# Performance work log

Hardware: AMD Instinct MI355X
Metric: run time of the kernel (lower is better)

Reference implementation:

```python
import jax, jax.numpy as jnp
import numpy as np

HIDDEN = 2048
NUM_HEADS = 16
HEAD_DIM = HIDDEN // NUM_HEADS  # 128
ROPE_THETA = 10000.0
T = 4096


def _rope(x, positions):
    # x: [T, H, D]; neox-style rotary (rotate halves), matching vLLM get_rope default
    half = HEAD_DIM // 2
    inv_freq = 1.0 / (ROPE_THETA ** (jnp.arange(0, half, dtype=jnp.float32) / half))
    freqs = positions.astype(jnp.float32)[:, None] * inv_freq[None, :]  # [T, half]
    cos = jnp.cos(freqs)[:, None, :]  # [T, 1, half]
    sin = jnp.sin(freqs)[:, None, :]
    x1, x2 = x[..., :half], x[..., half:]
    return jnp.concatenate([x1 * cos - x2 * sin, x2 * cos + x1 * sin], axis=-1)


def setup_inputs() -> dict:
    key = jax.random.key(0)
    k1, k2, k3 = jax.random.split(key, 3)
    return {
        "hidden_states": jax.random.normal(k1, (T, HIDDEN), dtype=jnp.float32),
        "positions": jnp.arange(T, dtype=jnp.int32),
        "w_qkv": jax.random.normal(k2, (HIDDEN, 3 * HIDDEN), dtype=jnp.float32) * (HIDDEN ** -0.5),
        "w_o": jax.random.normal(k3, (HIDDEN, HIDDEN), dtype=jnp.float32) * (HIDDEN ** -0.5),
    }


def reference(hidden_states, positions, w_qkv, w_o):
    qkv = hidden_states @ w_qkv  # [T, 3H]
    q, k, v = jnp.split(qkv, 3, axis=-1)
    q = q.reshape(T, NUM_HEADS, HEAD_DIM)
    k = k.reshape(T, NUM_HEADS, HEAD_DIM)
    v = v.reshape(T, NUM_HEADS, HEAD_DIM)
    q = _rope(q, positions)
    k = _rope(k, positions)
    scale = HEAD_DIM ** -0.5
    # causal SDPA over flattened single sequence
    scores = jnp.einsum("qhd,khd->hqk", q, k) * scale  # [H, T, T]
    causal = jnp.tril(jnp.ones((T, T), dtype=bool))
    scores = jnp.where(causal[None, :, :], scores, jnp.finfo(scores.dtype).min)
    probs = jax.nn.softmax(scores, axis=-1)
    attn = jnp.einsum("hqk,khd->qhd", probs, v).reshape(T, HIDDEN)
    return attn @ w_o
```

## Files before the change

### kernel.cpp

```cpp
#include <hip/hip_runtime.h>
#include <hip/hip_bf16.h>
#include <cstdint>
#include <cstddef>

#define T_SEQ 4096
#define HID   2048
#define NH    16
#define HD    128
#define QKVN  6144
#define KVB   32
#define CHT   16
#define CPH   144

typedef unsigned short u16;
typedef unsigned int u32;
typedef __bf16 bf16x8 __attribute__((ext_vector_type(8)));
typedef float  f32x4  __attribute__((ext_vector_type(4)));

typedef const __attribute__((address_space(1))) void* gas_ptr;
typedef __attribute__((address_space(3))) void* las_ptr;

__device__ __forceinline__ void async16(const void* g, void* l) {
  __builtin_amdgcn_global_load_lds((gas_ptr)g, (las_ptr)l, 16, 0, 0);
}

__device__ __forceinline__ u16 f2bf(float f) {
  unsigned int u = __float_as_uint(f);
  u += 0x7fffu + ((u >> 16) & 1u);
  return (u16)(u >> 16);
}

__device__ __forceinline__ float bf2f(u16 x) {
  return __uint_as_float((unsigned)x << 16);
}

__global__ void cast_f32_bf16(const float* __restrict__ in, u16* __restrict__ out, int n) {
  int i = (blockIdx.x * blockDim.x + threadIdx.x) * 4;
  if (i >= n) return;
  float4 v = *(const float4*)&in[i];
  uint2 o;
  o.x = (unsigned)f2bf(v.x) | ((unsigned)f2bf(v.y) << 16);
  o.y = (unsigned)f2bf(v.z) | ((unsigned)f2bf(v.w) << 16);
  *(uint2*)&out[i] = o;
}

__global__ void transpose_cast(const float* __restrict__ in, u16* __restrict__ out,
                               int R, int C) {
  __shared__ float tile[64][65];
  int c0 = blockIdx.x * 64, r0 = blockIdx.y * 64;
  int tid = threadIdx.x;
#pragma unroll
  for (int i = 0; i < 16; ++i) {
    int e = i * 256 + tid;
    int rr = e >> 6, cc = e & 63;
    tile[rr][cc] = in[(size_t)(r0 + rr) * C + c0 + cc];
  }
  __syncthreads();
#pragma unroll
  for (int i = 0; i < 16; ++i) {
    int e = i * 256 + tid;
    int oc = e >> 6, orr = e & 63;
    out[(size_t)(c0 + oc) * R + r0 + orr] = f2bf(tile[orr][oc]);
  }
}

template <typename OUT>
__global__ __launch_bounds__(256)
void gemm_bf16_bt(const u16* __restrict__ A, const u16* __restrict__ BT,
                  OUT* __restrict__ C, int M, int N, int K) {
  __shared__ u16 As[2][128 * 32];
  __shared__ u16 Bs[2][128 * 32];
  int tid = threadIdx.x;
  int row0 = blockIdx.y * 128, col0 = blockIdx.x * 128;
  int wv = tid >> 6, lane = tid & 63, lr = lane & 15, lq = lane >> 4;
  int wm = (wv >> 1) * 64, wn = (wv & 1) * 64;
  f32x4 acc[4][4] = {};

  auto stage = [&](int buf, int ks) {
#pragma unroll
    for (int k = 0; k < 2; ++k) {
      int c = k * 256 + tid;
      int row = c >> 2, col = c & 3;
      int key = (row >> 1) & 3;
      async16(&A[(size_t)(row0 + row) * K + ks + (col ^ key) * 8], &As[buf][c * 8]);
      async16(&BT[(size_t)(col0 + row) * K + ks + (col ^ key) * 8], &Bs[buf][c * 8]);
    }
  };

  stage(0, 0);
  __syncthreads();
  int nk = K >> 5;
  for (int t = 0; t < nk; ++t) {
    int cur = t & 1;
    if (t + 1 < nk) stage(cur ^ 1, (t + 1) * 32);

    const char* AsB = (const char*)&As[cur][0];
    const char* BsB = (const char*)&Bs[cur][0];
    bf16x8 a[4], b[4];
#pragma unroll
    for (int mi = 0; mi < 4; ++mi) {
      int row = wm + mi * 16 + lr;
      a[mi] = *(const bf16x8*)(AsB + row * 64 + ((lq ^ ((row >> 1) & 3)) << 4));
    }
#pragma unroll
    for (int ni = 0; ni < 4; ++ni) {
      int row = wn + ni * 16 + lr;
      b[ni] = *(const bf16x8*)(BsB + row * 64 + ((lq ^ ((row >> 1) & 3)) << 4));
    }
#pragma unroll
    for (int mi = 0; mi < 4; ++mi)
#pragma unroll
      for (int ni = 0; ni < 4; ++ni)
        acc[mi][ni] = __builtin_amdgcn_mfma_f32_16x16x32_bf16(a[mi], b[ni], acc[mi][ni], 0, 0, 0);
    __syncthreads();
  }

#pragma unroll
  for (int mi = 0; mi < 4; ++mi)
#pragma unroll
    for (int ni = 0; ni < 4; ++ni)
#pragma unroll
      for (int r = 0; r < 4; ++r) {
        float v = acc[mi][ni][r];
        size_t idx = (size_t)(row0 + wm + mi * 16 + lq * 4 + r) * N + col0 + wn + ni * 16 + lr;
        if constexpr (sizeof(OUT) == 2) C[idx] = (OUT)f2bf(v);
        else                            C[idx] = (OUT)v;
      }
}

#define SCL2 0.12753224f

__global__ void rope_reorg(const u16* __restrict__ qkv, const int* __restrict__ pos,
                           u16* __restrict__ Qh, u16* __restrict__ Kh) {
  int idx = blockIdx.x * 256 + threadIdx.x;
  if (idx >= T_SEQ * NH * 64) return;
  int d = idx & 63;
  int h = (idx >> 6) & (NH - 1);
  int t = idx >> 10;
  float p = (float)pos[t];
  float inv = exp2f((float)d * -0.20762050594046932f);
  float f = p * inv;
  float s, c;
  __sincosf(f, &s, &c);

  size_t ib = (size_t)t * QKVN + h * HD + d;
  float q1 = bf2f(qkv[ib]), q2 = bf2f(qkv[ib + 64]);
  float k1 = bf2f(qkv[ib + HID]), k2 = bf2f(qkv[ib + HID + 64]);
  size_t ob = ((size_t)h * T_SEQ + t) * HD + d;
  Qh[ob]      = f2bf((q1 * c - q2 * s) * SCL2);
  Qh[ob + 64] = f2bf((q2 * c + q1 * s) * SCL2);
  Kh[ob]      = f2bf(k1 * c - k2 * s);
  Kh[ob + 64] = f2bf(k2 * c + k1 * s);
}

__global__ void vtrans(const u16* __restrict__ qkv, u16* __restrict__ Vt) {
  __shared__ u16 tile[64][136];
  int t0 = blockIdx.x * 64;
  int h = blockIdx.y;
  int tid = threadIdx.x;
#pragma unroll
  for (int i = 0; i < 32; ++i) {
    int e = i * 256 + tid;
    int tt = e >> 7, d = e & 127;
    tile[tt][d] = qkv[(size_t)(t0 + tt) * QKVN + 2 * HID + h * HD + d];
  }
  __syncthreads();
#pragma unroll
  for (int i = 0; i < 32; ++i) {
    int e = i * 256 + tid;
    int d = e >> 6, tt = e & 63;
    Vt[((size_t)h * HD + d) * T_SEQ + t0 + tt] = tile[tt][d];
  }
}

__global__ __launch_bounds__(256)
void attn_fwd(const u16* __restrict__ Qh, const u16* __restrict__ Kh,
              const u16* __restrict__ Vt, u16* __restrict__ Opart,
              float2* __restrict__ ml) {
  __shared__ u16 Ks[2][32 * 128];
  __shared__ u16 Vs[2][128 * 32];
  __shared__ u16 Ps[4][32 * 32];

  int tid = threadIdx.x;
  int wv = tid >> 6, lane = tid & 63, lr = lane & 15, lq = lane >> 4;
  char* PsB = (char*)&Ps[wv][0];

  int id = blockIdx.x;
  int h = id / CPH;
  int w = id - h * CPH;
  int bq = 0, acc = 0;
  for (;;) {
    int ch = (bq + 4) >> 2;
    if (w < acc + ch) break;
    acc += ch;
    ++bq;
  }
  int c = w - acc;
  int nt = 4 * bq + 4;
  int j0 = c * CHT, j1 = min(j0 + CHT, nt);
  int q0 = bq * 128, wrow0 = q0 + wv * 32;

  bf16x8 qf[2][4];
#pragma unroll
  for (int qi = 0; qi < 2; ++qi)
#pragma unroll
    for (int kd = 0; kd < 4; ++kd)
      qf[qi][kd] = *(const bf16x8*)
          &Qh[((size_t)h * T_SEQ + wrow0 + qi * 16 + lr) * HD + kd * 32 + lq * 8];

  f32x4 acc_o[2][8] = {};
  float m_run[2] = {-1e30f, -1e30f};
  float l_run[2] = {0.0f, 0.0f};

  auto stage = [&](int buf, int jb) {
#pragma unroll
    for (int k = 0; k < 2; ++k) {
      int cc = k * 256 + tid;
      int row = cc >> 4;
      int sc = (cc ^ (row & 7)) & 15;
      async16(&Kh[((size_t)h * T_SEQ + jb + row) * HD + sc * 8], &Ks[buf][cc * 8]);
    }
#pragma unroll
    for (int k = 0; k < 2; ++k) {
      int cc = k * 256 + tid;
      int row = cc >> 2, col = cc & 3;
      int key = (row >> 1) & 3;
      async16(&Vt[((size_t)h * HD + row) * T_SEQ + jb + (col ^ key) * 8],
              &Vs[buf][cc * 8]);
    }
  };

  stage(0, j0 * KVB);
  __syncthreads();

  for (int j = j0; j < j1; ++j) {
    int cur = (j - j0) & 1;
    int jb = j * KVB;
    if (j + 1 < j1) stage(cur ^ 1, jb + KVB);

    if (jb <= wrow0 + 31) {
      const char* KsB = (const char*)&Ks[cur][0];
      const char* VsB = (const char*)&Vs[cur][0];

      f32x4 st[2][2] = {};
#pragma unroll
      for (int kd = 0; kd < 4; ++kd) {
#pragma unroll
        for (int kj = 0; kj < 2; ++kj) {
          int row = kj * 16 + lr;
          int byt = (row << 8) + kd * 64 + lq * 16;
          bf16x8 kf = *(const bf16x8*)(KsB + (byt ^ ((row & 7) << 4)));
#pragma unroll
          for (int qi = 0; qi < 2; ++qi)
            st[kj][qi] = __builtin_amdgcn_mfma_f32_16x16x32_bf16(
                kf, qf[qi][kd], st[kj][qi], 0, 0, 0);
        }
      }

      if (jb + KVB - 1 > wrow0) {
#pragma unroll
        for (int qi = 0; qi < 2; ++qi) {
          int qg = wrow0 + qi * 16 + lr;
#pragma unroll
          for (int kj = 0; kj < 2; ++kj)
#pragma unroll
            for (int r = 0; r < 4; ++r)
              if (jb + kj * 16 + lq * 4 + r > qg) st[kj][qi][r] = -1e30f;
        }
      }

      float sf[2];
#pragma unroll
      for (int qi = 0; qi < 2; ++qi) {
        float mx = fmaxf(fmaxf(fmaxf(st[0][qi][0], st[0][qi][1]),
                               fmaxf(st[0][qi][2], st[0][qi][3])),
                         fmaxf(fmaxf(st[1][qi][0], st[1][qi][1]),
                               fmaxf(st[1][qi][2], st[1][qi][3])));
        mx = fmaxf(mx, __shfl_xor(mx, 16));
        mx = fmaxf(mx, __shfl_xor(mx, 32));
        float mnew = fmaxf(m_run[qi], mx);
        sf[qi] = exp2f(m_run[qi] - mnew);
        m_run[qi] = mnew;

        int rowb = (qi * 16 + lr) * 64;
        int key = ((lr >> 1) & 3) << 4;
        float rs = 0.0f;
#pragma unroll
        for (int kj = 0; kj < 2; ++kj) {
          float p0 = exp2f(st[kj][qi][0] - mnew);
          float p1 = exp2f(st[kj][qi][1] - mnew);
          float p2 = exp2f(st[kj][qi][2] - mnew);
          float p3 = exp2f(st[kj][qi][3] - mnew);
          rs += (p0 + p1) + (p2 + p3);
          uint2 wq;
          wq.x = (u32)f2bf(p0) | ((u32)f2bf(p1) << 16);
          wq.y = (u32)f2bf(p2) | ((u32)f2bf(p3) << 16);
          *(uint2*)(PsB + rowb + (((kj * 16 + lq * 4) * 2) ^ key)) = wq;
        }
        l_run[qi] = l_run[qi] * sf[qi] + rs;
      }

#pragma unroll
      for (int mi = 0; mi < 2; ++mi) {
        float sfb[4];
#pragma unroll
        for (int r = 0; r < 4; ++r) sfb[r] = __shfl(sf[mi], lq * 4 + r);
#pragma unroll
        for (int nd = 0; nd < 8; ++nd)
#pragma unroll
          for (int r = 0; r < 4; ++r) acc_o[mi][nd][r] *= sfb[r];
      }

#pragma unroll
      for (int mi = 0; mi < 2; ++mi) {
        int prow = mi * 16 + lr;
        bf16x8 pa = *(const bf16x8*)(PsB + prow * 64 + ((lq ^ ((lr >> 1) & 3)) << 4));
#pragma unroll
        for (int nd = 0; nd < 8; ++nd) {
          int vrow = nd * 16 + lr;
          bf16x8 vb = *(const bf16x8*)(VsB + vrow * 64 + ((lq ^ ((vrow >> 1) & 3)) << 4));
          acc_o[mi][nd] = __builtin_amdgcn_mfma_f32_16x16x32_bf16(
              pa, vb, acc_o[mi][nd], 0, 0, 0);
        }
      }
    }
    __syncthreads();
  }

  u16* Op = Opart + (size_t)id * 128 * 128;
#pragma unroll
  for (int mi = 0; mi < 2; ++mi) {
    float l = l_run[mi];
    l += __shfl_xor(l, 16);
    l += __shfl_xor(l, 32);
    if (lq == 0) {
      int rowl = wv * 32 + mi * 16 + lr;
      ml[(size_t)id * 128 + rowl] = make_float2(m_run[mi], l);
    }
#pragma unroll
    for (int r = 0; r < 4; ++r) {
      int rowl = wv * 32 + mi * 16 + lq * 4 + r;
#pragma unroll
      for (int nd = 0; nd < 8; ++nd)
        Op[rowl * 128 + nd * 16 + lr] = f2bf(acc_o[mi][nd][r]);
    }
  }
}

__global__ __launch_bounds__(256)
void attn_combine(const u16* __restrict__ Opart, const float2* __restrict__ ml,
                  u16* __restrict__ attn) {
  int idx = blockIdx.x * 256 + threadIdx.x;
  int e8 = idx * 8;
  int qrow = e8 >> 11;
  int col = e8 & (HID - 1);
  int h = col >> 7, coll = col & 127;
  int bq = qrow >> 7, ql = qrow & 127;
  int a = bq >> 2, r = bq & 3;
  int base = h * CPH + (a + 1) * (2 * a + r);
  int n = (bq + 4) >> 2;

  float m = -1e30f;
  for (int c = 0; c < n; ++c) m = fmaxf(m, ml[(size_t)(base + c) * 128 + ql].x);
  float lsum = 0.0f;
  float o[8] = {};
  for (int c = 0; c < n; ++c) {
    float2 mlc = ml[(size_t)(base + c) * 128 + ql];
    float wgt = exp2f(mlc.x - m);
    lsum += mlc.y * wgt;
    const u16* src = Opart + ((size_t)(base + c) * 128 + ql) * 128 + coll;
    ushort4 v0 = *(const ushort4*)src;
    ushort4 v1 = *(const ushort4*)(src + 4);
    o[0] += bf2f(v0.x) * wgt; o[1] += bf2f(v0.y) * wgt;
    o[2] += bf2f(v0.z) * wgt; o[3] += bf2f(v0.w) * wgt;
    o[4] += bf2f(v1.x) * wgt; o[5] += bf2f(v1.y) * wgt;
    o[6] += bf2f(v1.z) * wgt; o[7] += bf2f(v1.w) * wgt;
  }
  float rl = 1.0f / lsum;
  uint4 w;
  w.x = (u32)f2bf(o[0] * rl) | ((u32)f2bf(o[1] * rl) << 16);
  w.y = (u32)f2bf(o[2] * rl) | ((u32)f2bf(o[3] * rl) << 16);
  w.z = (u32)f2bf(o[4] * rl) | ((u32)f2bf(o[5] * rl) << 16);
  w.w = (u32)f2bf(o[6] * rl) | ((u32)f2bf(o[7] * rl) << 16);
  *(uint4*)&attn[e8] = w;
}

extern "C" void kernel_launch(void* const* d_in, const int* in_sizes, int n_in,
                              void* d_out, int out_size, void* d_ws, size_t ws_size,
                              hipStream_t stream) {
  const float* hidden    = (const float*)d_in[0];
  const int*   positions = (const int*)d_in[1];
  const float* w_qkv     = (const float*)d_in[2];
  const float* w_o       = (const float*)d_in[3];
  float* out = (float*)d_out;

  char* p = (char*)d_ws;
  u16* woT    = (u16*)p;  p += (size_t)HID * HID * 2;
  u16* Qh     = (u16*)p;  p += (size_t)T_SEQ * HID * 2;
  u16* Kh     = (u16*)p;  p += (size_t)T_SEQ * HID * 2;
  u16* Vt     = (u16*)p;  p += (size_t)T_SEQ * HID * 2;
  u16* attn_b = (u16*)p;  p += (size_t)T_SEQ * HID * 2;
  char* un = p;
  u16* hs_b   = (u16*)un;
  u16* wqkvT  = (u16*)(un + (size_t)T_SEQ * HID * 2);
  u16* qkvb   = (u16*)(un + (size_t)T_SEQ * HID * 2 + (size_t)QKVN * HID * 2);
  u16* Opart  = (u16*)un;
  float2* ml  = (float2*)(un + (size_t)NH * CPH * 128 * 128 * 2);

  cast_f32_bf16<<<(T_SEQ * HID / 4 + 255) / 256, 256, 0, stream>>>(hidden, hs_b, T_SEQ * HID);
  transpose_cast<<<dim3(QKVN / 64, HID / 64), 256, 0, stream>>>(w_qkv, wqkvT, HID, QKVN);
  transpose_cast<<<dim3(HID / 64, HID / 64), 256, 0, stream>>>(w_o, woT, HID, HID);
  gemm_bf16_bt<u16><<<dim3(QKVN / 128, T_SEQ / 128), 256, 0, stream>>>(hs_b, wqkvT, qkvb,
                                                                       T_SEQ, QKVN, HID);
  rope_reorg<<<(T_SEQ * NH * 64 + 255) / 256, 256, 0, stream>>>(qkvb, positions, Qh, Kh);
  vtrans<<<dim3(T_SEQ / 64, NH), 256, 0, stream>>>(qkvb, Vt);
  attn_fwd<<<NH * CPH, 256, 0, stream>>>(Qh, Kh, Vt, Opart, ml);
  attn_combine<<<T_SEQ * HID / 8 / 256, 256, 0, stream>>>(Opart, ml, attn_b);
  gemm_bf16_bt<float><<<dim3(HID / 128, T_SEQ / 128), 256, 0, stream>>>(attn_b, woT, out,
                                                                        T_SEQ, HID, HID);
}
```

Before: 416.3 us.

## Compute transposed PV accumulators to drop rescale shuffles and skip unneeded rescaling

Swaps the MFMA operand order in the P·V product so each lane's accumulator holds output columns for its own query row. The online-softmax rescale factor can then be applied directly without per-row shuffles. The rescale is skipped when no lane's running max changed, and the stores become packed 4-element bf16 writes. It also uses native bf16 conversions for packing P, which adds a wave-wide vote branch and changes the output register layout.

```diff
diff --git a/kernel.cpp b/kernel.cpp
--- a/kernel.cpp
+++ b/kernel.cpp
@@ -15,6 +15,7 @@
 typedef unsigned short u16;
 typedef unsigned int u32;
 typedef __bf16 bf16x8 __attribute__((ext_vector_type(8)));
+typedef __bf16 bf16x4 __attribute__((ext_vector_type(4)));
 typedef float  f32x4  __attribute__((ext_vector_type(4)));
 
 typedef const __attribute__((address_space(1))) void* gas_ptr;
@@ -208,7 +209,7 @@
       qf[qi][kd] = *(const bf16x8*)
           &Qh[((size_t)h * T_SEQ + wrow0 + qi * 16 + lr) * HD + kd * 32 + lq * 8];
 
-  f32x4 acc_o[2][8] = {};
+  f32x4 acc_ot[8][2] = {};
   float m_run[2] = {-1e30f, -1e30f};
   float l_run[2] = {0.0f, 0.0f};
 
@@ -292,36 +293,37 @@
           float p2 = exp2f(st[kj][qi][2] - mnew);
           float p3 = exp2f(st[kj][qi][3] - mnew);
           rs += (p0 + p1) + (p2 + p3);
-          uint2 wq;
-          wq.x = (u32)f2bf(p0) | ((u32)f2bf(p1) << 16);
-          wq.y = (u32)f2bf(p2) | ((u32)f2bf(p3) << 16);
-          *(uint2*)(PsB + rowb + (((kj * 16 + lq * 4) * 2) ^ key)) = wq;
+          bf16x4 pk;
+          pk[0] = (__bf16)p0; pk[1] = (__bf16)p1;
+          pk[2] = (__bf16)p2; pk[3] = (__bf16)p3;
+          *(bf16x4*)(PsB + rowb + (((kj * 16 + lq * 4) * 2) ^ key)) = pk;
         }
         l_run[qi] = l_run[qi] * sf[qi] + rs;
       }
 
-#pragma unroll
-      for (int mi = 0; mi < 2; ++mi) {
-        float sfb[4];
-#pragma unroll
-        for (int r = 0; r < 4; ++r) sfb[r] = __shfl(sf[mi], lq * 4 + r);
-#pragma unroll
-        for (int nd = 0; nd < 8; ++nd)
-#pragma unroll
-          for (int r = 0; r < 4; ++r) acc_o[mi][nd][r] *= sfb[r];
-      }
-
-#pragma unroll
-      for (int mi = 0; mi < 2; ++mi) {
-        int prow = mi * 16 + lr;
-        bf16x8 pa = *(const bf16x8*)(PsB + prow * 64 + ((lq ^ ((lr >> 1) & 3)) << 4));
-#pragma unroll
-        for (int nd = 0; nd < 8; ++nd) {
-          int vrow = nd * 16 + lr;
-          bf16x8 vb = *(const bf16x8*)(VsB + vrow * 64 + ((lq ^ ((vrow >> 1) & 3)) << 4));
-          acc_o[mi][nd] = __builtin_amdgcn_mfma_f32_16x16x32_bf16(
-              pa, vb, acc_o[mi][nd], 0, 0, 0);
-        }
+      if (__any((sf[0] < 1.0f) || (sf[1] < 1.0f))) {
+#pragma unroll
+        for (int di = 0; di < 8; ++di)
+#pragma unroll
+          for (int qi = 0; qi < 2; ++qi)
+#pragma unroll
+            for (int r = 0; r < 4; ++r) acc_ot[di][qi][r] *= sf[qi];
+      }
+
+      bf16x8 pa[2];
+#pragma unroll
+      for (int qi = 0; qi < 2; ++qi) {
+        int prow = qi * 16 + lr;
+        pa[qi] = *(const bf16x8*)(PsB + prow * 64 + ((lq ^ ((lr >> 1) & 3)) << 4));
+      }
+#pragma unroll
+      for (int di = 0; di < 8; ++di) {
+        int vrow = di * 16 + lr;
+        bf16x8 vb = *(const bf16x8*)(VsB + vrow * 64 + ((lq ^ ((vrow >> 1) & 3)) << 4));
+#pragma unroll
+        for (int qi = 0; qi < 2; ++qi)
+          acc_ot[di][qi] = __builtin_amdgcn_mfma_f32_16x16x32_bf16(
+              vb, pa[qi], acc_ot[di][qi], 0, 0, 0);
       }
     }
     __syncthreads();
@@ -329,20 +331,20 @@
 
   u16* Op = Opart + (size_t)id * 128 * 128;
 #pragma unroll
-  for (int mi = 0; mi < 2; ++mi) {
-    float l = l_run[mi];
+  for (int qi = 0; qi < 2; ++qi) {
+    float l = l_run[qi];
     l += __shfl_xor(l, 16);
     l += __shfl_xor(l, 32);
-    if (lq == 0) {
-      int rowl = wv * 32 + mi * 16 + lr;
-      ml[(size_t)id * 128 + rowl] = make_float2(m_run[mi], l);
-    }
-#pragma unroll
-    for (int r = 0; r < 4; ++r) {
-      int rowl = wv * 32 + mi * 16 + lq * 4 + r;
-#pragma unroll
-      for (int nd = 0; nd < 8; ++nd)
-        Op[rowl * 128 + nd * 16 + lr] = f2bf(acc_o[mi][nd][r]);
+    int q = wv * 32 + qi * 16 + lr;
+    if (lq == 0) ml[(size_t)id * 128 + q] = make_float2(m_run[qi], l);
+#pragma unroll
+    for (int di = 0; di < 8; ++di) {
+      bf16x4 pk;
+      pk[0] = (__bf16)acc_ot[di][qi][0];
+      pk[1] = (__bf16)acc_ot[di][qi][1];
+      pk[2] = (__bf16)acc_ot[di][qi][2];
+      pk[3] = (__bf16)acc_ot[di][qi][3];
+      *(bf16x4*)&Op[q * 128 + di * 16 + lq * 4] = pk;
     }
   }
 }
```

Result: no change. 419.6 us (+0.8%).
